# Kernel tuning notes

Measured on AMD Instinct MI355X. Metric: run time of the kernel, lower is better.

Reference implementation:

```python
import jax, jax.numpy as jnp
import numpy as np

HEADS = 8
D = 1024


def setup_inputs() -> dict:
    key = jax.random.key(0)
    ks = jax.random.split(key, 10)
    B, Sq, Sk = 8, 2048, 2048
    x = jax.random.normal(ks[0], (B, Sq, D), dtype=jnp.float32)
    context = jax.random.normal(ks[1], (B, Sk, D), dtype=jnp.float32)
    # Dense params (glorot-ish scale)
    def dense(k, fin, fout):
        return jax.random.normal(k, (fin, fout), dtype=jnp.float32) / np.sqrt(fin)
    Wq = dense(ks[2], D, HEADS); bq = jnp.zeros((HEADS,), jnp.float32)
    Wk = dense(ks[3], D, HEADS); bk = jnp.zeros((HEADS,), jnp.float32)
    Wv = dense(ks[4], D, HEADS); bv = jnp.zeros((HEADS,), jnp.float32)
    Wo = dense(ks[5], HEADS, D); bo = jnp.zeros((D,), jnp.float32)
    return {"x": x, "context": context, "Wq": Wq, "bq": bq,
            "Wk": Wk, "bk": bk, "Wv": Wv, "bv": bv, "Wo": Wo, "bo": bo}


def reference(x, context, Wq, bq, Wk, bk, Wv, bv, Wo, bo):
    # q: [B,Sq,H], k/v: [B,Sk,H]  (H = heads = projection width, no head split)
    q = jnp.einsum('bsd,dh->bsh', x, Wq) + bq
    k = jnp.einsum('btd,dh->bth', context, Wk) + bk
    v = jnp.einsum('btd,dh->bth', context, Wv) + bv
    # Dot(axes=-1): scores[b,s,t] = q[b,s,:] . k[b,t,:]  -> [B,Sq,Sk]
    scores = jnp.einsum('bsh,bth->bst', q, k)
    weights = jax.nn.softmax(scores, axis=-1)  # no 1/sqrt(d) scaling in original
    # Dot(axes=(-1,1)): out[b,s,h] = sum_t weights[b,s,t] * v[b,t,h]
    out = jnp.einsum('bst,bth->bsh', weights, v)
    return jnp.einsum('bsh,hd->bsd', out, Wo) + bo
```

## Files before the change

kernel.cpp:

```cpp
#include <hip/hip_runtime.h>

constexpr int D = 1024;
constexpr int H = 8;
constexpr int S = 2048;
constexpr int B = 8;
constexpr int NROW = B * S;

__device__ __forceinline__ int swz(int i) { return i ^ ((i >> 3) & 7); }

__global__ __launch_bounds__(512)
void proj_kernel(const float* __restrict__ x, const float* __restrict__ ctx,
                 const float* __restrict__ Wq, const float* __restrict__ bq,
                 const float* __restrict__ Wk, const float* __restrict__ bk,
                 const float* __restrict__ Wv, const float* __restrict__ bv,
                 float* __restrict__ qo, float* __restrict__ ko,
                 float* __restrict__ vo)
{
    __shared__ float4 wlds[2048];
    const int tid = threadIdx.x;
    const int bid = (int)blockIdx.x;
    const int tensor = (bid >> 3) % 3;
    const int blk    = (bid / 24) * 8 + (bid & 7);

    const float* W    = (tensor == 0) ? Wq : (tensor == 1) ? Wk : Wv;
    const float* bias = (tensor == 0) ? bq : (tensor == 1) ? bk : bv;
    const float* src  = (tensor == 0) ? x  : ctx;
    float*       dst  = (tensor == 0) ? qo : (tensor == 1) ? ko : vo;

    {
        const float4* w4 = (const float4*)W;
        for (int i = tid; i < 2048; i += 512) wlds[swz(i)] = w4[i];
    }
    __syncthreads();

    const int c    = tid & 15;
    const int team = tid >> 4;
    const int row0 = blk * 64 + team * 2;
    const float4* r0 = (const float4*)(src + (size_t)row0 * D);
    const float4* r1 = (const float4*)(src + (size_t)(row0 + 1) * D);

    float a0[8], a1[8];
#pragma unroll
    for (int h = 0; h < 8; ++h) { a0[h] = 0.f; a1[h] = 0.f; }

#pragma unroll 4
    for (int j = 0; j < 16; ++j) {
        const float4 xa = r0[16 * j + c];
        const float4 xb = r1[16 * j + c];
        const int ib = 128 * j + 8 * c;
#pragma unroll
        for (int e = 0; e < 4; ++e) {
            const float4 w0 = wlds[swz(ib + 2 * e)];
            const float4 w1 = wlds[swz(ib + 2 * e + 1)];
            const float s0 = (&xa.x)[e], s1 = (&xb.x)[e];
            a0[0] += s0 * w0.x; a0[1] += s0 * w0.y; a0[2] += s0 * w0.z; a0[3] += s0 * w0.w;
            a0[4] += s0 * w1.x; a0[5] += s0 * w1.y; a0[6] += s0 * w1.z; a0[7] += s0 * w1.w;
            a1[0] += s1 * w0.x; a1[1] += s1 * w0.y; a1[2] += s1 * w0.z; a1[3] += s1 * w0.w;
            a1[4] += s1 * w1.x; a1[5] += s1 * w1.y; a1[6] += s1 * w1.z; a1[7] += s1 * w1.w;
        }
    }

#pragma unroll
    for (int h = 0; h < 8; ++h) {
        float s0 = a0[h], s1 = a1[h];
        s0 += __shfl_down(s0, 8); s1 += __shfl_down(s1, 8);
        s0 += __shfl_down(s0, 4); s1 += __shfl_down(s1, 4);
        s0 += __shfl_down(s0, 2); s1 += __shfl_down(s1, 2);
        s0 += __shfl_down(s0, 1); s1 += __shfl_down(s1, 1);
        if (c == 0) {
            dst[(size_t)row0 * H + h]       = s0 + bias[h];
            dst[(size_t)(row0 + 1) * H + h] = s1 + bias[h];
        }
    }
}

constexpr int RPW = 4;
constexpr int RPB = 16;
constexpr int TILE_T = 512;

__global__ __launch_bounds__(256)
void attn_kernel(const float* __restrict__ q, const float* __restrict__ k,
                 const float* __restrict__ v, const float* __restrict__ Wo,
                 const float* __restrict__ bo, float* __restrict__ out)
{
    __shared__ float4 ka[TILE_T], kb[TILE_T];
    __shared__ float4 va[TILE_T], vb[TILE_T];
    const int tid  = threadIdx.x;
    const int lane = tid & 63;
    const int wid  = tid >> 6;

    const int row0 = blockIdx.x * RPB + wid * RPW;
    const int b = row0 >> 11;

    float qv[RPW][H];
#pragma unroll
    for (int r = 0; r < RPW; ++r) {
        const float4* q4 = (const float4*)(q + (size_t)(row0 + r) * H);
        const float4 a = q4[0], c = q4[1];
        qv[r][0] = a.x; qv[r][1] = a.y; qv[r][2] = a.z; qv[r][3] = a.w;
        qv[r][4] = c.x; qv[r][5] = c.y; qv[r][6] = c.z; qv[r][7] = c.w;
    }

    float l[RPW] = {0.f, 0.f, 0.f, 0.f};
    float o[RPW][H];
#pragma unroll
    for (int r = 0; r < RPW; ++r)
#pragma unroll
        for (int h = 0; h < H; ++h) o[r][h] = 0.f;

    const float4* kg = (const float4*)(k + (size_t)b * S * H);
    const float4* vg = (const float4*)(v + (size_t)b * S * H);

    for (int tile = 0; tile < S / TILE_T; ++tile) {
        __syncthreads();
#pragma unroll
        for (int i = 0; i < TILE_T / 256; ++i) {
            const int t = i * 256 + tid;
            const int g = tile * TILE_T + t;
            ka[t] = kg[2 * g];  kb[t] = kg[2 * g + 1];
            va[t] = vg[2 * g];  vb[t] = vg[2 * g + 1];
        }
        __syncthreads();

        float4 k0 = ka[lane], k1 = kb[lane];
        float4 v0 = va[lane], v1 = vb[lane];
#pragma unroll
        for (int m = 0; m < TILE_T / 64; ++m) {
            float4 nk0, nk1, nv0, nv1;
            if (m + 1 < TILE_T / 64) {
                const int t = lane + ((m + 1) << 6);
                nk0 = ka[t]; nk1 = kb[t]; nv0 = va[t]; nv1 = vb[t];
            }
#pragma unroll
            for (int r = 0; r < RPW; ++r) {
                const float s = qv[r][0] * k0.x + qv[r][1] * k0.y
                              + qv[r][2] * k0.z + qv[r][3] * k0.w
                              + qv[r][4] * k1.x + qv[r][5] * k1.y
                              + qv[r][6] * k1.z + qv[r][7] * k1.w;
                const float e = __expf(s);
                l[r] += e;
                o[r][0] += e * v0.x; o[r][1] += e * v0.y;
                o[r][2] += e * v0.z; o[r][3] += e * v0.w;
                o[r][4] += e * v1.x; o[r][5] += e * v1.y;
                o[r][6] += e * v1.z; o[r][7] += e * v1.w;
            }
            if (m + 1 < TILE_T / 64) {
                k0 = nk0; k1 = nk1; v0 = nv0; v1 = nv1;
            }
        }
    }

#pragma unroll
    for (int r = 0; r < RPW; ++r) {
#pragma unroll
        for (int off = 32; off > 0; off >>= 1) l[r] += __shfl_xor(l[r], off);
        const float inv = 1.f / l[r];
#pragma unroll
        for (int h = 0; h < H; ++h) {
#pragma unroll
            for (int off = 32; off > 0; off >>= 1) o[r][h] += __shfl_xor(o[r][h], off);
            o[r][h] *= inv;
        }
    }

    const float4* Wo4 = (const float4*)Wo;
    const float4* bo4 = (const float4*)bo;
    float4* out4 = (float4*)out;
#pragma unroll
    for (int c = 0; c < 4; ++c) {
        const int f = lane + 64 * c;
        float4 w[H];
#pragma unroll
        for (int h = 0; h < H; ++h) w[h] = Wo4[h * (D / 4) + f];
        const float4 base = bo4[f];
#pragma unroll
        for (int r = 0; r < RPW; ++r) {
            float4 acc = base;
#pragma unroll
            for (int h = 0; h < H; ++h) {
                acc.x += o[r][h] * w[h].x;
                acc.y += o[r][h] * w[h].y;
                acc.z += o[r][h] * w[h].z;
                acc.w += o[r][h] * w[h].w;
            }
            out4[(size_t)(row0 + r) * (D / 4) + f] = acc;
        }
    }
}

extern "C" void kernel_launch(void* const* d_in, const int* in_sizes, int n_in,
                              void* d_out, int out_size, void* d_ws, size_t ws_size,
                              hipStream_t stream) {
    const float* x   = (const float*)d_in[0];
    const float* ctx = (const float*)d_in[1];
    const float* Wq  = (const float*)d_in[2];
    const float* bq  = (const float*)d_in[3];
    const float* Wk  = (const float*)d_in[4];
    const float* bk  = (const float*)d_in[5];
    const float* Wv  = (const float*)d_in[6];
    const float* bv  = (const float*)d_in[7];
    const float* Wo  = (const float*)d_in[8];
    const float* bo  = (const float*)d_in[9];
    float* out = (float*)d_out;

    float* qw = (float*)d_ws;
    float* kw = qw + (size_t)NROW * H;
    float* vw = kw + (size_t)NROW * H;

    proj_kernel<<<dim3(3 * NROW / 64), dim3(512), 0, stream>>>(
        x, ctx, Wq, bq, Wk, bk, Wv, bv, qw, kw, vw);
    attn_kernel<<<dim3(NROW / RPB), dim3(256), 0, stream>>>(
        qw, kw, vw, Wo, bo, out);
}
```

Baseline: 234.3 us.

## Restructure projection kernel to stage x tiles in LDS with wave-uniform weight reads

```diff
diff --git a/kernel.cpp b/kernel.cpp
--- a/kernel.cpp
+++ b/kernel.cpp
@@ -6,9 +6,7 @@
 constexpr int B = 8;
 constexpr int NROW = B * S;
 
-__device__ __forceinline__ int swz(int i) { return i ^ ((i >> 3) & 7); }
-
-__global__ __launch_bounds__(512)
+__global__ __launch_bounds__(256)
 void proj_kernel(const float* __restrict__ x, const float* __restrict__ ctx,
                  const float* __restrict__ Wq, const float* __restrict__ bq,
                  const float* __restrict__ Wk, const float* __restrict__ bk,
@@ -16,8 +14,14 @@
                  float* __restrict__ qo, float* __restrict__ ko,
                  float* __restrict__ vo)
 {
-    __shared__ float4 wlds[2048];
-    const int tid = threadIdx.x;
+    __shared__ float4 xt[32 * 64];
+    __shared__ float  red[4 * 64 * 8];
+
+    const int tid   = threadIdx.x;
+    const int lane  = tid & 63;
+    const int wid_v = tid >> 6;
+    const int wid   = __builtin_amdgcn_readfirstlane(wid_v);
+
     const int bid = (int)blockIdx.x;
     const int tensor = (bid >> 3) % 3;
     const int blk    = (bid / 24) * 8 + (bid & 7);
@@ -27,51 +31,61 @@
     const float* src  = (tensor == 0) ? x  : ctx;
     float*       dst  = (tensor == 0) ? qo : (tensor == 1) ? ko : vo;
 
-    {
-        const float4* w4 = (const float4*)W;
-        for (int i = tid; i < 2048; i += 512) wlds[swz(i)] = w4[i];
-    }
+    const int row0 = blk * 64;
+    const float4* x4 = (const float4*)src + (size_t)row0 * 256;
+
+    float acc[8];
+#pragma unroll
+    for (int h = 0; h < 8; ++h) acc[h] = 0.f;
+
+    const int sk4    = tid & 31;
+    const int srow_b = tid >> 5;
+
+    for (int chunk = 0; chunk < 8; ++chunk) {
+        __syncthreads();
+#pragma unroll
+        for (int p = 0; p < 8; ++p) {
+            const int srow = p * 8 + srow_b;
+            xt[sk4 * 64 + (srow ^ (sk4 & 7))] =
+                x4[(size_t)srow * 256 + chunk * 32 + sk4];
+        }
+        __syncthreads();
+
+#pragma unroll 4
+        for (int i = 0; i < 8; ++i) {
+            const int k4 = wid * 8 + i;
+            const float4 xv = xt[k4 * 64 + (lane ^ (k4 & 7))];
+            const float* Wb = W + ((size_t)chunk * 128 + k4 * 4) * 8;
+#pragma unroll
+            for (int e = 0; e < 4; ++e) {
+                const float xs = (&xv.x)[e];
+                acc[0] += xs * Wb[e * 8 + 0];
+                acc[1] += xs * Wb[e * 8 + 1];
+                acc[2] += xs * Wb[e * 8 + 2];
+                acc[3] += xs * Wb[e * 8 + 3];
+                acc[4] += xs * Wb[e * 8 + 4];
+                acc[5] += xs * Wb[e * 8 + 5];
+                acc[6] += xs * Wb[e * 8 + 6];
+                acc[7] += xs * Wb[e * 8 + 7];
+            }
+        }
+    }
+
+    float4* red4 = (float4*)red;
+    red4[wid_v * 128 + lane * 2 + 0] = make_float4(acc[0], acc[1], acc[2], acc[3]);
+    red4[wid_v * 128 + lane * 2 + 1] = make_float4(acc[4], acc[5], acc[6], acc[7]);
     __syncthreads();
 
-    const int c    = tid & 15;
-    const int team = tid >> 4;
-    const int row0 = blk * 64 + team * 2;
-    const float4* r0 = (const float4*)(src + (size_t)row0 * D);
-    const float4* r1 = (const float4*)(src + (size_t)(row0 + 1) * D);
-
-    float a0[8], a1[8];
-#pragma unroll
-    for (int h = 0; h < 8; ++h) { a0[h] = 0.f; a1[h] = 0.f; }
-
-#pragma unroll 4
-    for (int j = 0; j < 16; ++j) {
-        const float4 xa = r0[16 * j + c];
-        const float4 xb = r1[16 * j + c];
-        const int ib = 128 * j + 8 * c;
-#pragma unroll
-        for (int e = 0; e < 4; ++e) {
-            const float4 w0 = wlds[swz(ib + 2 * e)];
-            const float4 w1 = wlds[swz(ib + 2 * e + 1)];
-            const float s0 = (&xa.x)[e], s1 = (&xb.x)[e];
-            a0[0] += s0 * w0.x; a0[1] += s0 * w0.y; a0[2] += s0 * w0.z; a0[3] += s0 * w0.w;
-            a0[4] += s0 * w1.x; a0[5] += s0 * w1.y; a0[6] += s0 * w1.z; a0[7] += s0 * w1.w;
-            a1[0] += s1 * w0.x; a1[1] += s1 * w0.y; a1[2] += s1 * w0.z; a1[3] += s1 * w0.w;
-            a1[4] += s1 * w1.x; a1[5] += s1 * w1.y; a1[6] += s1 * w1.z; a1[7] += s1 * w1.w;
-        }
-    }
-
-#pragma unroll
-    for (int h = 0; h < 8; ++h) {
-        float s0 = a0[h], s1 = a1[h];
-        s0 += __shfl_down(s0, 8); s1 += __shfl_down(s1, 8);
-        s0 += __shfl_down(s0, 4); s1 += __shfl_down(s1, 4);
-        s0 += __shfl_down(s0, 2); s1 += __shfl_down(s1, 2);
-        s0 += __shfl_down(s0, 1); s1 += __shfl_down(s1, 1);
-        if (c == 0) {
-            dst[(size_t)row0 * H + h]       = s0 + bias[h];
-            dst[(size_t)(row0 + 1) * H + h] = s1 + bias[h];
-        }
-    }
+    const int oi   = tid * 2;
+    const int orow = oi >> 3;
+    const int oh   = oi & 7;
+    float s0 = bias[oh], s1 = bias[oh + 1];
+#pragma unroll
+    for (int w = 0; w < 4; ++w) {
+        s0 += red[w * 512 + orow * 8 + oh];
+        s1 += red[w * 512 + orow * 8 + oh + 1];
+    }
+    *(float2*)(dst + (size_t)(row0 + orow) * H + oh) = make_float2(s0, s1);
 }
 
 constexpr int RPW = 4;
@@ -207,7 +221,7 @@
     float* kw = qw + (size_t)NROW * H;
     float* vw = kw + (size_t)NROW * H;
 
-    proj_kernel<<<dim3(3 * NROW / 64), dim3(512), 0, stream>>>(
+    proj_kernel<<<dim3(3 * NROW / 64), dim3(256), 0, stream>>>(
         x, ctx, Wq, bq, Wk, bk, Wv, bv, qw, kw, vw);
     attn_kernel<<<dim3(NROW / RPB), dim3(256), 0, stream>>>(
         qw, kw, vw, Wo, bo, out);
```

After: 230.6 us. Within noise of the previous version (-1.6%).
